# Kernel tuning notes

Hardware: AMD Instinct MI355X
Metric: run time of the kernel (lower is better)

The kernel has to match this reference:

```python
import jax, jax.numpy as jnp
import numpy as np

N_A, N_B = 30000, 30000
V, D_IN, D_OUT, H, E = 2, 128, 128, 4, 480000
EPS_LN = 1e-5


def setup_inputs() -> dict:
    key = jax.random.key(0)
    ks = jax.random.split(key, 22)
    rn = lambda i, sh, s=1.0: jax.random.normal(ks[i], sh, dtype=jnp.float32) * s
    ri = lambda i, n: jax.random.randint(ks[i], (E,), 0, n, dtype=jnp.int32)
    return {
        'feat_A': rn(0, (N_A, V, D_IN)),
        'feat_B': rn(1, (N_B, V, D_IN)),
        'src_ab': ri(2, N_A), 'dst_ab': ri(3, N_B),
        'val_ab': jax.random.uniform(ks[4], (E,), dtype=jnp.float32),
        'src_ba': ri(5, N_B), 'dst_ba': ri(6, N_A),
        'val_ba': jax.random.uniform(ks[7], (E,), dtype=jnp.float32),
        'W1': rn(8, (D_OUT, D_IN), 0.05), 'b1': jnp.zeros((D_OUT,), jnp.float32),
        'g1': jnp.ones((D_OUT,), jnp.float32), 'be1': jnp.zeros((D_OUT,), jnp.float32),
        'W2': rn(9, (D_OUT, D_IN), 0.05), 'b2': jnp.zeros((D_OUT,), jnp.float32),
        'g2': jnp.ones((D_OUT,), jnp.float32), 'be2': jnp.zeros((D_OUT,), jnp.float32),
        'Win': rn(10, (3 * D_OUT, D_OUT), 0.05), 'bin_': jnp.zeros((3 * D_OUT,), jnp.float32),
        'Wout': rn(11, (D_OUT, D_OUT), 0.05), 'bout': jnp.zeros((D_OUT,), jnp.float32),
        'lng': jnp.ones((D_OUT,), jnp.float32), 'lnb': jnp.zeros((D_OUT,), jnp.float32),
    }


def spmm_t(src, dst, val, h, n_out):
    # (adj^T @ h) over all views: h [N_src, V, d] -> [n_out, V, d]
    msg = h[src] * val[:, None, None]
    return jax.ops.segment_sum(msg, dst, num_segments=n_out)


def l2norm(x):
    n = jnp.sqrt(jnp.sum(x * x, axis=-1, keepdims=True))
    return x / jnp.maximum(n, 1e-12)


def layernorm(x, g, b):
    mu = jnp.mean(x, axis=-1, keepdims=True)
    var = jnp.mean((x - mu) ** 2, axis=-1, keepdims=True)
    return (x - mu) * jax.lax.rsqrt(var + EPS_LN) * g + b


def proj(x, W, b, g, be):
    # Linear -> LayerNorm -> ReLU
    return jax.nn.relu(layernorm(x @ W.T + b, g, be))


def mha(x, Win, bin_, Wout, bout, num_heads):
    # self-attention over the metapath axis P; x [..., P, d]
    *lead, P, d = x.shape
    dh = d // num_heads
    q, k, v = jnp.split(x @ Win.T + bin_, 3, axis=-1)
    hd = lambda t: t.reshape(*lead, P, num_heads, dh)
    q = hd(q) * (dh ** -0.5)
    scores = jnp.einsum('...qhe,...khe->...hqk', q, hd(k))
    a = jax.nn.softmax(scores, axis=-1)
    o = jnp.einsum('...hqk,...khe->...qhe', a, hd(v)).reshape(*lead, P, d)
    return o @ Wout.T + bout


def reference(feat_A, feat_B, src_ab, dst_ab, val_ab, src_ba, dst_ba, val_ba,
              W1, b1, g1, be1, W2, b2, g2, be2, Win, bin_, Wout, bout, lng, lnb):
    # metapath A->B->A
    h = l2norm(spmm_t(src_ab, dst_ab, val_ab, feat_A, N_B))
    h = l2norm(spmm_t(src_ba, dst_ba, val_ba, h, N_A))
    h1 = proj(h, W1, b1, g1, be1)                       # [N_A, V, d]
    # metapath B->A
    h = l2norm(spmm_t(src_ba, dst_ba, val_ba, feat_B, N_A))
    h2 = proj(h, W2, b2, g2, be2)                       # [N_A, V, d]
    x = jnp.stack([h1, h2], axis=2)                     # [N_A, V, P=2, d]
    attn = mha(x, Win, bin_, Wout, bout, H)
    y = layernorm(attn + x, lng, lnb).mean(axis=2)      # [N_A, V, d]
    return y  # h_global['A']; type B is identity passthrough of feat_B
```

## Files before the change

### kernel.cpp

```cpp
#include <hip/hip_runtime.h>

#define D 128
#define NODE_ROW 256
#define AP 8
#define AR (AP * 2)

typedef __attribute__((ext_vector_type(8))) short short8;
typedef __attribute__((ext_vector_type(4))) float floatx4;

__device__ __forceinline__ ushort f2bf(float f) {
    unsigned int u = __float_as_uint(f);
    u += 0x7fffu + ((u >> 16) & 1u);
    return (ushort)(u >> 16);
}
__device__ __forceinline__ unsigned int pk2(float a, float b) {
    return (unsigned int)f2bf(a) | ((unsigned int)f2bf(b) << 16);
}
__device__ __forceinline__ void up8(uint4 u, float* f) {
    f[0] = __uint_as_float(u.x << 16); f[1] = __uint_as_float(u.x & 0xffff0000u);
    f[2] = __uint_as_float(u.y << 16); f[3] = __uint_as_float(u.y & 0xffff0000u);
    f[4] = __uint_as_float(u.z << 16); f[5] = __uint_as_float(u.z & 0xffff0000u);
    f[6] = __uint_as_float(u.w << 16); f[7] = __uint_as_float(u.w & 0xffff0000u);
}
__device__ __forceinline__ float bf2f(ushort h) {
    return __uint_as_float(((unsigned int)h) << 16);
}
__device__ __forceinline__ short8 ldfrag(const ushort* p) {
    union { uint4 u; short8 s; } cv;
    cv.u = *(const uint4*)p;
    return cv.s;
}
__device__ __forceinline__ void acc4(float4& a, float w, uint2 u) {
    a.x += w * __uint_as_float(u.x << 16);
    a.y += w * __uint_as_float(u.x & 0xffff0000u);
    a.z += w * __uint_as_float(u.y << 16);
    a.w += w * __uint_as_float(u.y & 0xffff0000u);
}

__global__ __launch_bounds__(256) void k_f2b2(
    const float* __restrict__ srcA, const float* __restrict__ srcB,
    ushort* __restrict__ dstA, ushort* __restrict__ dstB, int n8) {
    int i = blockIdx.x * 256 + threadIdx.x;
    const float* s; ushort* d; int k;
    if (i < n8) { s = srcA; d = dstA; k = i; }
    else if (i < 2 * n8) { s = srcB; d = dstB; k = i - n8; }
    else return;
    const float4* sp = (const float4*)s + (size_t)k * 2;
    float4 a = sp[0], b = sp[1];
    uint4 o;
    o.x = pk2(a.x, a.y); o.y = pk2(a.z, a.w);
    o.z = pk2(b.x, b.y); o.w = pk2(b.z, b.w);
    ((uint4*)d)[k] = o;
}


__global__ __launch_bounds__(256) void k_hist(
    const int* __restrict__ dst_ab, const int* __restrict__ dst_ba,
    int* __restrict__ cnt_ab, int* __restrict__ cnt_ba, int E) {
    int i = blockIdx.x * 256 + threadIdx.x;
    if (i >= E) return;
    atomicAdd(&cnt_ab[dst_ab[i]], 1);
    atomicAdd(&cnt_ba[dst_ba[i]], 1);
}

__global__ __launch_bounds__(1024) void k_scan2(
    int* __restrict__ cntB, int* __restrict__ startB, int nB_,
    int* __restrict__ cntA, int* __restrict__ startA, int nA_) {
    __shared__ int part[1024];
    int* cnt; int* start; int n;
    if (blockIdx.x == 0) { cnt = cntB; start = startB; n = nB_; }
    else                 { cnt = cntA; start = startA; n = nA_; }
    int t = threadIdx.x;
    int chunk = (n + 1023) >> 10;
    int lo = min(t * chunk, n), hi = min(lo + chunk, n);
    int s = 0;
    for (int i = lo; i < hi; i++) s += cnt[i];
    part[t] = s;
    __syncthreads();
    for (int d = 1; d < 1024; d <<= 1) {
        int v = (t >= d) ? part[t - d] : 0;
        __syncthreads();
        part[t] += v;
        __syncthreads();
    }
    int off = part[t] - s;
    for (int i = lo; i < hi; i++) {
        int c = cnt[i];
        start[i] = off;
        cnt[i] = off;
        off += c;
    }
    if (t == 1023) start[n] = off;
}

__global__ __launch_bounds__(256) void k_scatter(
    const int* __restrict__ src_ab, const int* __restrict__ dst_ab,
    const float* __restrict__ val_ab,
    const int* __restrict__ src_ba, const int* __restrict__ dst_ba,
    const float* __restrict__ val_ba,
    int* __restrict__ cur_ab, int* __restrict__ cur_ba,
    int2* __restrict__ ep_ab, int2* __restrict__ ep_ba, int E) {
    int i = blockIdx.x * 256 + threadIdx.x;
    if (i >= E) return;
    {
        int pos = atomicAdd(&cur_ab[dst_ab[i]], 1);
        ep_ab[pos] = make_int2(src_ab[i], __float_as_int(val_ab[i]));
    }
    {
        int pos = atomicAdd(&cur_ba[dst_ba[i]], 1);
        ep_ba[pos] = make_int2(src_ba[i], __float_as_int(val_ba[i]));
    }
}


__global__ __launch_bounds__(256) void k_gather_norm_bf(
    const ushort* __restrict__ feat, const int2* __restrict__ ep,
    const int* __restrict__ start, ushort* __restrict__ out, int n) {
    int node = blockIdx.x * 4 + (threadIdx.x >> 6);
    if (node >= n) return;
    int lane = threadIdx.x & 63;
    int lo = start[node], hi = start[node + 1];
    float4 acc = make_float4(0.f, 0.f, 0.f, 0.f);
    int i = lo;
    for (; i + 3 < hi; i += 4) {
        int2 p0 = ep[i], p1 = ep[i + 1], p2 = ep[i + 2], p3 = ep[i + 3];
        uint2 u0 = ((const uint2*)(feat + (size_t)p0.x * NODE_ROW))[lane];
        uint2 u1 = ((const uint2*)(feat + (size_t)p1.x * NODE_ROW))[lane];
        uint2 u2 = ((const uint2*)(feat + (size_t)p2.x * NODE_ROW))[lane];
        uint2 u3 = ((const uint2*)(feat + (size_t)p3.x * NODE_ROW))[lane];
        acc4(acc, __int_as_float(p0.y), u0);
        acc4(acc, __int_as_float(p1.y), u1);
        acc4(acc, __int_as_float(p2.y), u2);
        acc4(acc, __int_as_float(p3.y), u3);
    }
    for (; i < hi; i++) {
        int2 p = ep[i];
        uint2 u = ((const uint2*)(feat + (size_t)p.x * NODE_ROW))[lane];
        acc4(acc, __int_as_float(p.y), u);
    }
    float ss = acc.x * acc.x + acc.y * acc.y + acc.z * acc.z + acc.w * acc.w;
    #pragma unroll
    for (int o = 16; o > 0; o >>= 1) ss += __shfl_xor(ss, o, 32);
    float sc = 1.0f / fmaxf(sqrtf(ss), 1e-12f);
    uint2 o;
    o.x = pk2(acc.x * sc, acc.y * sc);
    o.y = pk2(acc.z * sc, acc.w * sc);
    ((uint2*)(out + (size_t)node * NODE_ROW))[lane] = o;
}

__global__ __launch_bounds__(256) void k_gather2_bf(
    const ushort* __restrict__ featP, const ushort* __restrict__ featQ,
    const int2* __restrict__ ep, const int* __restrict__ start,
    ushort* __restrict__ outP, ushort* __restrict__ outQ, int n) {
    int node = blockIdx.x * 4 + (threadIdx.x >> 6);
    if (node >= n) return;
    int lane = threadIdx.x & 63;
    int lo = start[node], hi = start[node + 1];
    float4 aP = make_float4(0.f, 0.f, 0.f, 0.f);
    float4 aQ = make_float4(0.f, 0.f, 0.f, 0.f);
    int i = lo;
    for (; i + 3 < hi; i += 4) {
        int2 p0 = ep[i], p1 = ep[i + 1], p2 = ep[i + 2], p3 = ep[i + 3];
        size_t o0 = (size_t)p0.x * NODE_ROW, o1 = (size_t)p1.x * NODE_ROW;
        size_t o2 = (size_t)p2.x * NODE_ROW, o3 = (size_t)p3.x * NODE_ROW;
        uint2 uP0 = ((const uint2*)(featP + o0))[lane];
        uint2 uQ0 = ((const uint2*)(featQ + o0))[lane];
        uint2 uP1 = ((const uint2*)(featP + o1))[lane];
        uint2 uQ1 = ((const uint2*)(featQ + o1))[lane];
        uint2 uP2 = ((const uint2*)(featP + o2))[lane];
        uint2 uQ2 = ((const uint2*)(featQ + o2))[lane];
        uint2 uP3 = ((const uint2*)(featP + o3))[lane];
        uint2 uQ3 = ((const uint2*)(featQ + o3))[lane];
        float w0 = __int_as_float(p0.y), w1 = __int_as_float(p1.y);
        float w2 = __int_as_float(p2.y), w3 = __int_as_float(p3.y);
        acc4(aP, w0, uP0); acc4(aQ, w0, uQ0);
        acc4(aP, w1, uP1); acc4(aQ, w1, uQ1);
        acc4(aP, w2, uP2); acc4(aQ, w2, uQ2);
        acc4(aP, w3, uP3); acc4(aQ, w3, uQ3);
    }
    for (; i < hi; i++) {
        int2 p = ep[i];
        float w = __int_as_float(p.y);
        size_t off = (size_t)p.x * NODE_ROW;
        uint2 uP = ((const uint2*)(featP + off))[lane];
        uint2 uQ = ((const uint2*)(featQ + off))[lane];
        acc4(aP, w, uP); acc4(aQ, w, uQ);
    }
    uint2 oP, oQ;
    oP.x = pk2(aP.x, aP.y); oP.y = pk2(aP.z, aP.w);
    oQ.x = pk2(aQ.x, aQ.y); oQ.y = pk2(aQ.z, aQ.w);
    ((uint2*)(outP + (size_t)node * NODE_ROW))[lane] = oP;
    ((uint2*)(outQ + (size_t)node * NODE_ROW))[lane] = oQ;
}

__global__ __launch_bounds__(256) void k_cvt(
    const float* __restrict__ W1, const float* __restrict__ W2,
    const float* __restrict__ Win, const float* __restrict__ Wout,
    ushort* __restrict__ dst) {
    int idx = (blockIdx.x * 256 + threadIdx.x) * 4;
    if (idx >= 98304) return;
    const float* s; int off;
    if (idx < 16384)      { s = W1;  off = idx; }
    else if (idx < 32768) { s = W2;  off = idx - 16384; }
    else if (idx < 81920) { s = Win; off = idx - 32768; }
    else                  { s = Wout; off = idx - 81920; }
    float4 f = *(const float4*)(s + off);
    uint2 p;
    p.x = pk2(f.x, f.y);
    p.y = pk2(f.z, f.w);
    *(uint2*)(dst + idx) = p;
}

__global__ __launch_bounds__(128) void k_projm2(
    const ushort* __restrict__ in1, const ushort* __restrict__ Wb1,
    const float* __restrict__ b1, const float* __restrict__ g1,
    const float* __restrict__ be1,
    const ushort* __restrict__ in2, const ushort* __restrict__ Wb2,
    const float* __restrict__ b2, const float* __restrict__ g2,
    const float* __restrict__ be2,
    ushort* __restrict__ xbuf) {
    __shared__ ushort xn[16][136];
    __shared__ float yb[16][128];
    int p = blockIdx.y;
    const ushort* in = p ? in2 : in1;
    const ushort* Wb = p ? Wb2 : Wb1;
    const float*  b  = p ? b2  : b1;
    const float*  g  = p ? g2  : g1;
    const float*  be = p ? be2 : be1;
    int t = threadIdx.x;
    size_t rowbase = (size_t)blockIdx.x * 16;
    int r = t >> 3, i = t & 7;

    {
        const ushort* gp = in + (rowbase + r) * D + i * 16;
        float v[16];
        up8(((const uint4*)gp)[0], v);
        up8(((const uint4*)gp)[1], v + 8);
        float ss = 0.f;
        #pragma unroll
        for (int e = 0; e < 16; e++) ss += v[e] * v[e];
        ss += __shfl_xor(ss, 1, 8);
        ss += __shfl_xor(ss, 2, 8);
        ss += __shfl_xor(ss, 4, 8);
        float sc = 1.0f / fmaxf(sqrtf(ss), 1e-12f);
        uint4 w0, w1;
        w0.x = pk2(v[0]*sc, v[1]*sc);   w0.y = pk2(v[2]*sc, v[3]*sc);
        w0.z = pk2(v[4]*sc, v[5]*sc);   w0.w = pk2(v[6]*sc, v[7]*sc);
        w1.x = pk2(v[8]*sc, v[9]*sc);   w1.y = pk2(v[10]*sc, v[11]*sc);
        w1.z = pk2(v[12]*sc, v[13]*sc); w1.w = pk2(v[14]*sc, v[15]*sc);
        ushort* dst = &xn[r][i * 16];
        ((uint4*)dst)[0] = w0;
        ((uint4*)dst)[1] = w1;
    }
    __syncthreads();

    {
        int lane = t & 63, w = t >> 6, c = lane & 15, quad = lane >> 4;
        short8 af[4];
        #pragma unroll
        for (int kt = 0; kt < 4; kt++)
            af[kt] = ldfrag(&xn[c][kt * 32 + quad * 8]);
        #pragma unroll
        for (int nt2 = 0; nt2 < 4; nt2++) {
            int j = (w * 4 + nt2) * 16 + c;
            floatx4 acc = {0.f, 0.f, 0.f, 0.f};
            #pragma unroll
            for (int kt = 0; kt < 4; kt++) {
                short8 bfr = ldfrag(Wb + (size_t)j * 128 + kt * 32 + quad * 8);
                acc = __builtin_amdgcn_mfma_f32_16x16x32_bf16(af[kt], bfr, acc, 0, 0, 0);
            }
            float bj = b[j];
            #pragma unroll
            for (int rg = 0; rg < 4; rg++)
                yb[quad * 4 + rg][j] = acc[rg] + bj;
        }
    }
    __syncthreads();

    {
        float v[16];
        const float* yr = &yb[r][i * 16];
        #pragma unroll
        for (int e = 0; e < 16; e++) v[e] = yr[e];
        float s1 = 0.f, s2 = 0.f;
        #pragma unroll
        for (int e = 0; e < 16; e++) { s1 += v[e]; s2 += v[e] * v[e]; }
        s1 += __shfl_xor(s1, 1, 8); s2 += __shfl_xor(s2, 1, 8);
        s1 += __shfl_xor(s1, 2, 8); s2 += __shfl_xor(s2, 2, 8);
        s1 += __shfl_xor(s1, 4, 8); s2 += __shfl_xor(s2, 4, 8);
        float mu = s1 * (1.0f / 128.0f);
        float var = s2 * (1.0f / 128.0f) - mu * mu;
        float rs = rsqrtf(var + 1e-5f);
        const float* gg = g + i * 16;
        const float* bb = be + i * 16;
        float res[16];
        #pragma unroll
        for (int e = 0; e < 16; e++)
            res[e] = fmaxf((v[e] - mu) * rs * gg[e] + bb[e], 0.f);
        ushort* op = xbuf + ((rowbase + r) * 2 + p) * D + i * 16;
        uint4 w0, w1;
        w0.x = pk2(res[0], res[1]);   w0.y = pk2(res[2], res[3]);
        w0.z = pk2(res[4], res[5]);   w0.w = pk2(res[6], res[7]);
        w1.x = pk2(res[8], res[9]);   w1.y = pk2(res[10], res[11]);
        w1.z = pk2(res[12], res[13]); w1.w = pk2(res[14], res[15]);
        ((uint4*)op)[0] = w0;
        ((uint4*)op)[1] = w1;
    }
}

#define QKS 260
__global__ __launch_bounds__(256, 5) void k_attn2(
    const ushort* __restrict__ xbuf,
    const ushort* __restrict__ Winb, const float* __restrict__ binq,
    const ushort* __restrict__ Woutb, const float* __restrict__ bout,
    const float* __restrict__ lng, const float* __restrict__ lnb,
    float* __restrict__ out) {
    __shared__ ushort xb[AR][136];
    __shared__ float qk[AR][QKS];
    __shared__ ushort vb[AR][136];
    __shared__ ushort ob[AR][136];
    __shared__ float mu_s[AR], rs_s[AR];
    int t = threadIdx.x;
    int lane = t & 63, w = t >> 6;
    int c = lane & 15, quad = lane >> 4;
    size_t pairbase = (size_t)blockIdx.x * AP;
    size_t rowbase = pairbase * 2;

    const uint2* gx = (const uint2*)(xbuf + rowbase * D);
    #pragma unroll
    for (int i = t; i < AR * D / 4; i += 256) {
        int r = i >> 5;
        int col = (i & 31) * 4;
        *(uint2*)&xb[r][col] = gx[i];
    }
    __syncthreads();

    {
        short8 af[4];
        #pragma unroll
        for (int kt = 0; kt < 4; kt++)
            af[kt] = ldfrag(&xb[c][kt * 32 + quad * 8]);
        #pragma unroll
        for (int nt2 = 0; nt2 < 6; nt2++) {
            int j = (w * 6 + nt2) * 16 + c;
            floatx4 acc = {0.f, 0.f, 0.f, 0.f};
            #pragma unroll
            for (int kt = 0; kt < 4; kt++) {
                short8 bfr = ldfrag(Winb + (size_t)j * 128 + kt * 32 + quad * 8);
                acc = __builtin_amdgcn_mfma_f32_16x16x32_bf16(af[kt], bfr, acc, 0, 0, 0);
            }
            float bj = binq[j];
            if (j < 256) {
                float sc = (j < 128) ? 0.17677669529663687f : 1.0f;
                #pragma unroll
                for (int rg = 0; rg < 4; rg++)
                    qk[quad * 4 + rg][j] = (acc[rg] + bj) * sc;
            } else {
                #pragma unroll
                for (int rg = 0; rg < 4; rg++)
                    vb[quad * 4 + rg][j - 256] = f2bf(acc[rg] + bj);
            }
        }
    }
    __syncthreads();

    {
        int half = t & 1, kk = (t >> 1) & 1, pq = (t >> 2) & 1;
        int h = (t >> 3) & 3, pp = t >> 5;
        int qrow = 2 * pp + pq;
        const float4* qp = (const float4*)&qk[qrow][h * 32 + half * 16];
        const float4* kp = (const float4*)&qk[2 * pp + kk][128 + h * 32 + half * 16];
        float s = 0.f;
        #pragma unroll
        for (int m = 0; m < 4; m++) {
            float4 qv = qp[m], kv = kp[m];
            s += qv.x * kv.x + qv.y * kv.y + qv.z * kv.z + qv.w * kv.w;
        }
        s += __shfl_xor(s, 1, 64);
        float so = __shfl_xor(s, 2, 64);
        float s0 = kk ? so : s;
        float s1 = kk ? s : so;
        float m0 = fmaxf(s0, s1);
        float e0 = __expf(s0 - m0), e1 = __expf(s1 - m0);
        float inv = 1.f / (e0 + e1);
        float a0 = e0 * inv, a1 = e1 * inv;
        int cbase = h * 32 + kk * 16 + half * 8;
        const uint2* v0p = (const uint2*)&vb[2 * pp][cbase];
        const uint2* v1p = (const uint2*)&vb[2 * pp + 1][cbase];
        ushort* op = &ob[qrow][cbase];
        #pragma unroll
        for (int m = 0; m < 2; m++) {
            uint2 u0 = v0p[m], u1 = v1p[m];
            float o0 = a0 * __uint_as_float(u0.x << 16)         + a1 * __uint_as_float(u1.x << 16);
            float o1 = a0 * __uint_as_float(u0.x & 0xffff0000u) + a1 * __uint_as_float(u1.x & 0xffff0000u);
            float o2 = a0 * __uint_as_float(u0.y << 16)         + a1 * __uint_as_float(u1.y << 16);
            float o3 = a0 * __uint_as_float(u0.y & 0xffff0000u) + a1 * __uint_as_float(u1.y & 0xffff0000u);
            uint2 pw;
            pw.x = pk2(o0, o1); pw.y = pk2(o2, o3);
            ((uint2*)op)[m] = pw;
        }
    }
    __syncthreads();

    {
        short8 af[4];
        #pragma unroll
        for (int kt = 0; kt < 4; kt++)
            af[kt] = ldfrag(&ob[c][kt * 32 + quad * 8]);
        #pragma unroll
        for (int nt2 = 0; nt2 < 2; nt2++) {
            int j = (w * 2 + nt2) * 16 + c;
            floatx4 acc = {0.f, 0.f, 0.f, 0.f};
            #pragma unroll
            for (int kt = 0; kt < 4; kt++) {
                short8 bfr = ldfrag(Woutb + (size_t)j * 128 + kt * 32 + quad * 8);
                acc = __builtin_amdgcn_mfma_f32_16x16x32_bf16(af[kt], bfr, acc, 0, 0, 0);
            }
            float bj = bout[j];
            #pragma unroll
            for (int rg = 0; rg < 4; rg++) {
                int row = quad * 4 + rg;
                qk[row][j] = acc[rg] + bj + bf2f(xb[row][j]);
            }
        }
    }
    __syncthreads();

    if (t < 128) {
        int r = t >> 3, i = t & 7;
        float s1 = 0.f, s2 = 0.f;
        const float* yr = &qk[r][i * 16];
        #pragma unroll
        for (int cc = 0; cc < 16; cc++) { float v = yr[cc]; s1 += v; s2 += v * v; }
        s1 += __shfl_down(s1, 4, 8); s2 += __shfl_down(s2, 4, 8);
        s1 += __shfl_down(s1, 2, 8); s2 += __shfl_down(s2, 2, 8);
        s1 += __shfl_down(s1, 1, 8); s2 += __shfl_down(s2, 1, 8);
        if (i == 0) {
            float mu = s1 / D;
            float var = s2 / D - mu * mu;
            mu_s[r] = mu; rs_s[r] = rsqrtf(var + 1e-5f);
        }
    }
    __syncthreads();

    if (t < 128) {
        int j = t;
        float gj = lng[j], bj = lnb[j];
        #pragma unroll
        for (int pp = 0; pp < AP; pp++) {
            int r0 = pp * 2, r1 = r0 + 1;
            float v0 = (qk[r0][j] - mu_s[r0]) * rs_s[r0] * gj + bj;
            float v1 = (qk[r1][j] - mu_s[r1]) * rs_s[r1] * gj + bj;
            out[(pairbase + pp) * D + j] = 0.5f * (v0 + v1);
        }
    }
}

extern "C" void kernel_launch(void* const* d_in, const int* in_sizes, int n_in,
                              void* d_out, int out_size, void* d_ws, size_t ws_size,
                              hipStream_t stream) {
    const float* feat_A = (const float*)d_in[0];
    const float* feat_B = (const float*)d_in[1];
    const int*   src_ab = (const int*)d_in[2];
    const int*   dst_ab = (const int*)d_in[3];
    const float* val_ab = (const float*)d_in[4];
    const int*   src_ba = (const int*)d_in[5];
    const int*   dst_ba = (const int*)d_in[6];
    const float* val_ba = (const float*)d_in[7];
    const float* W1 = (const float*)d_in[8];
    const float* b1 = (const float*)d_in[9];
    const float* g1 = (const float*)d_in[10];
    const float* be1 = (const float*)d_in[11];
    const float* W2 = (const float*)d_in[12];
    const float* b2 = (const float*)d_in[13];
    const float* g2 = (const float*)d_in[14];
    const float* be2 = (const float*)d_in[15];
    const float* Win = (const float*)d_in[16];
    const float* binq = (const float*)d_in[17];
    const float* Wout = (const float*)d_in[18];
    const float* bout = (const float*)d_in[19];
    const float* lng = (const float*)d_in[20];
    const float* lnb = (const float*)d_in[21];

    int E  = in_sizes[2];
    int nA = in_sizes[0] / NODE_ROW;
    int nB = in_sizes[1] / NODE_ROW;
    int rowsA = nA * 2;
    size_t nodeElems = (size_t)nA * NODE_ROW;

    ushort* fbA  = (ushort*)d_ws;
    ushort* fbB  = fbA + nodeElems;
    ushort* hB   = fbB + nodeElems;
    ushort* hA1  = hB + nodeElems;
    ushort* hA2  = hA1 + nodeElems;
    ushort* xbuf = hA2 + nodeElems;
    ushort* Wbf  = xbuf + (size_t)rowsA * 2 * D;
    ushort* W1b   = Wbf;
    ushort* W2b   = Wbf + 16384;
    ushort* Winb  = Wbf + 32768;
    ushort* Woutb = Wbf + 81920;
    int* cnt_ab   = (int*)(Wbf + 98304);
    int* cnt_ba   = cnt_ab + nB;
    int* start_ab = cnt_ba + nA;
    int* start_ba = start_ab + (nB + 1);
    uintptr_t a = (uintptr_t)(start_ba + (nA + 1));
    a = (a + 15) & ~(uintptr_t)15;
    int2* ep_ab = (int2*)a;
    int2* ep_ba = ep_ab + E;

    int egrid = (E + 255) / 256;
    int n8 = (int)(nodeElems / 8);

    k_f2b2<<<(2 * n8 + 255) / 256, 256, 0, stream>>>(feat_A, feat_B, fbA, fbB, n8);

    hipMemsetAsync(cnt_ab, 0, (size_t)(nA + nB) * sizeof(int), stream);
    k_hist<<<egrid, 256, 0, stream>>>(dst_ab, dst_ba, cnt_ab, cnt_ba, E);
    k_scan2<<<2, 1024, 0, stream>>>(cnt_ab, start_ab, nB, cnt_ba, start_ba, nA);
    k_scatter<<<egrid, 256, 0, stream>>>(src_ab, dst_ab, val_ab,
                                         src_ba, dst_ba, val_ba,
                                         cnt_ab, cnt_ba, ep_ab, ep_ba, E);

    k_cvt<<<96, 256, 0, stream>>>(W1, W2, Win, Wout, Wbf);

    k_gather_norm_bf<<<(nB + 3) / 4, 256, 0, stream>>>(fbA, ep_ab, start_ab, hB, nB);
    k_gather2_bf<<<(nA + 3) / 4, 256, 0, stream>>>(hB, fbB, ep_ba, start_ba,
                                                   hA1, hA2, nA);

    k_projm2<<<dim3(rowsA / 16, 2), 128, 0, stream>>>(hA1, W1b, b1, g1, be1,
                                                      hA2, W2b, b2, g2, be2, xbuf);
    k_attn2<<<rowsA / AP, 256, 0, stream>>>(xbuf, Winb, binq, Woutb, bout,
                                            lng, lnb, (float*)d_out);
}
```

Before: 560.7 us.

## Fuse attention scores and softmax into QKV MFMA registers in k_attn2

Each wave now computes the Q, K and V column tiles for the same head-aligned 32 columns, so the attention scores, the two-way softmax and the weighted sum over V are done directly from the MFMA accumulators with shuffle reductions. This removes the qk and vb shared staging buffers and one block barrier. The smaller shared-memory footprint allows a higher launch-bounds occupancy target (6 instead of 5). The cost is more live registers and extra cross-lane shuffles. V is also no longer rounded to bf16 before the weighted sum.

```diff
diff --git a/kernel.cpp b/kernel.cpp
--- a/kernel.cpp
+++ b/kernel.cpp
@@ -308,17 +308,15 @@
     }
 }
 
-#define QKS 260
-__global__ __launch_bounds__(256, 5) void k_attn2(
+__global__ __launch_bounds__(256, 6) void k_attn2(
     const ushort* __restrict__ xbuf,
     const ushort* __restrict__ Winb, const float* __restrict__ binq,
     const ushort* __restrict__ Woutb, const float* __restrict__ bout,
     const float* __restrict__ lng, const float* __restrict__ lnb,
     float* __restrict__ out) {
     __shared__ ushort xb[AR][136];
-    __shared__ float qk[AR][QKS];
-    __shared__ ushort vb[AR][136];
-    __shared__ ushort ob[AR][136];
+    __shared__ ushort obuf[AR][140];
+    __shared__ float yy[AR][132];
     __shared__ float mu_s[AR], rs_s[AR];
     int t = threadIdx.x;
     int lane = t & 63, w = t >> 6;
@@ -340,64 +338,66 @@
         #pragma unroll
         for (int kt = 0; kt < 4; kt++)
             af[kt] = ldfrag(&xb[c][kt * 32 + quad * 8]);
-        #pragma unroll
-        for (int nt2 = 0; nt2 < 6; nt2++) {
-            int j = (w * 6 + nt2) * 16 + c;
-            floatx4 acc = {0.f, 0.f, 0.f, 0.f};
+        floatx4 aq0 = {0.f,0.f,0.f,0.f}, aq1 = {0.f,0.f,0.f,0.f};
+        floatx4 ak0 = {0.f,0.f,0.f,0.f}, ak1 = {0.f,0.f,0.f,0.f};
+        floatx4 av0 = {0.f,0.f,0.f,0.f}, av1 = {0.f,0.f,0.f,0.f};
+        int jb = w * 32 + c;
+        #pragma unroll
+        for (int kt = 0; kt < 4; kt++) {
+            const ushort* wp = Winb + kt * 32 + quad * 8;
+            short8 f0 = ldfrag(wp + (size_t)(jb)       * 128);
+            short8 f1 = ldfrag(wp + (size_t)(jb + 16)  * 128);
+            short8 f2 = ldfrag(wp + (size_t)(jb + 128) * 128);
+            short8 f3 = ldfrag(wp + (size_t)(jb + 144) * 128);
+            short8 f4 = ldfrag(wp + (size_t)(jb + 256) * 128);
+            short8 f5 = ldfrag(wp + (size_t)(jb + 272) * 128);
+            aq0 = __builtin_amdgcn_mfma_f32_16x16x32_bf16(af[kt], f0, aq0, 0, 0, 0);
+            aq1 = __builtin_amdgcn_mfma_f32_16x16x32_bf16(af[kt], f1, aq1, 0, 0, 0);
+            ak0 = __builtin_amdgcn_mfma_f32_16x16x32_bf16(af[kt], f2, ak0, 0, 0, 0);
+            ak1 = __builtin_amdgcn_mfma_f32_16x16x32_bf16(af[kt], f3, ak1, 0, 0, 0);
+            av0 = __builtin_amdgcn_mfma_f32_16x16x32_bf16(af[kt], f4, av0, 0, 0, 0);
+            av1 = __builtin_amdgcn_mfma_f32_16x16x32_bf16(af[kt], f5, av1, 0, 0, 0);
+        }
+        const float qs = 0.17677669529663687f;
+        float bq0 = binq[jb] ;        float bq1 = binq[jb + 16];
+        float bk0 = binq[jb + 128];   float bk1 = binq[jb + 144];
+        float bv0 = binq[jb + 256];   float bv1 = binq[jb + 272];
+        #pragma unroll
+        for (int rg = 0; rg < 4; rg++) {
+            aq0[rg] = (aq0[rg] + bq0) * qs;
+            aq1[rg] = (aq1[rg] + bq1) * qs;
+            ak0[rg] += bk0;  ak1[rg] += bk1;
+            av0[rg] += bv0;  av1[rg] += bv1;
+        }
+        #pragma unroll
+        for (int pl = 0; pl < 2; pl++) {
+            int r0 = 2 * pl, r1 = 2 * pl + 1;
+            float p00 = aq0[r0] * ak0[r0] + aq1[r0] * ak1[r0];
+            float p01 = aq0[r0] * ak0[r1] + aq1[r0] * ak1[r1];
+            float p10 = aq0[r1] * ak0[r0] + aq1[r1] * ak1[r0];
+            float p11 = aq0[r1] * ak0[r1] + aq1[r1] * ak1[r1];
             #pragma unroll
-            for (int kt = 0; kt < 4; kt++) {
-                short8 bfr = ldfrag(Winb + (size_t)j * 128 + kt * 32 + quad * 8);
-                acc = __builtin_amdgcn_mfma_f32_16x16x32_bf16(af[kt], bfr, acc, 0, 0, 0);
+            for (int m = 1; m < 16; m <<= 1) {
+                p00 += __shfl_xor(p00, m, 16);
+                p01 += __shfl_xor(p01, m, 16);
+                p10 += __shfl_xor(p10, m, 16);
+                p11 += __shfl_xor(p11, m, 16);
             }
-            float bj = binq[j];
-            if (j < 256) {
-                float sc = (j < 128) ? 0.17677669529663687f : 1.0f;
-                #pragma unroll
-                for (int rg = 0; rg < 4; rg++)
-                    qk[quad * 4 + rg][j] = (acc[rg] + bj) * sc;
-            } else {
-                #pragma unroll
-                for (int rg = 0; rg < 4; rg++)
-                    vb[quad * 4 + rg][j - 256] = f2bf(acc[rg] + bj);
-            }
-        }
-    }
-    __syncthreads();
-
-    {
-        int half = t & 1, kk = (t >> 1) & 1, pq = (t >> 2) & 1;
-        int h = (t >> 3) & 3, pp = t >> 5;
-        int qrow = 2 * pp + pq;
-        const float4* qp = (const float4*)&qk[qrow][h * 32 + half * 16];
-        const float4* kp = (const float4*)&qk[2 * pp + kk][128 + h * 32 + half * 16];
-        float s = 0.f;
-        #pragma unroll
-        for (int m = 0; m < 4; m++) {
-            float4 qv = qp[m], kv = kp[m];
-            s += qv.x * kv.x + qv.y * kv.y + qv.z * kv.z + qv.w * kv.w;
-        }
-        s += __shfl_xor(s, 1, 64);
-        float so = __shfl_xor(s, 2, 64);
-        float s0 = kk ? so : s;
-        float s1 = kk ? s : so;
-        float m0 = fmaxf(s0, s1);
-        float e0 = __expf(s0 - m0), e1 = __expf(s1 - m0);
-        float inv = 1.f / (e0 + e1);
-        float a0 = e0 * inv, a1 = e1 * inv;
-        int cbase = h * 32 + kk * 16 + half * 8;
-        const uint2* v0p = (const uint2*)&vb[2 * pp][cbase];
-        const uint2* v1p = (const uint2*)&vb[2 * pp + 1][cbase];
-        ushort* op = &ob[qrow][cbase];
-        #pragma unroll
-        for (int m = 0; m < 2; m++) {
-            uint2 u0 = v0p[m], u1 = v1p[m];
-            float o0 = a0 * __uint_as_float(u0.x << 16)         + a1 * __uint_as_float(u1.x << 16);
-            float o1 = a0 * __uint_as_float(u0.x & 0xffff0000u) + a1 * __uint_as_float(u1.x & 0xffff0000u);
-            float o2 = a0 * __uint_as_float(u0.y << 16)         + a1 * __uint_as_float(u1.y << 16);
-            float o3 = a0 * __uint_as_float(u0.y & 0xffff0000u) + a1 * __uint_as_float(u1.y & 0xffff0000u);
-            uint2 pw;
-            pw.x = pk2(o0, o1); pw.y = pk2(o2, o3);
-            ((uint2*)op)[m] = pw;
+            float mx0 = fmaxf(p00, p01), mx1 = fmaxf(p10, p11);
+            float e00 = __expf(p00 - mx0), e01 = __expf(p01 - mx0);
+            float e10 = __expf(p10 - mx1), e11 = __expf(p11 - mx1);
+            float i0 = 1.f / (e00 + e01), i1 = 1.f / (e10 + e11);
+            float a00 = e00 * i0, a01 = e01 * i0;
+            float a10 = e10 * i1, a11 = e11 * i1;
+            float o00 = a00 * av0[r0] + a01 * av0[r1];
+            float o10 = a10 * av0[r0] + a11 * av0[r1];
+            float o01 = a00 * av1[r0] + a01 * av1[r1];
+            float o11 = a10 * av1[r0] + a11 * av1[r1];
+            int row0 = quad * 4 + r0, row1 = quad * 4 + r1;
+            obuf[row0][jb]      = f2bf(o00);
+            obuf[row1][jb]      = f2bf(o10);
+            obuf[row0][jb + 16] = f2bf(o01);
+            obuf[row1][jb + 16] = f2bf(o11);
         }
     }
     __syncthreads();
@@ -406,7 +406,7 @@
         short8 af[4];
         #pragma unroll
         for (int kt = 0; kt < 4; kt++)
-            af[kt] = ldfrag(&ob[c][kt * 32 + quad * 8]);
+            af[kt] = ldfrag(&obuf[c][kt * 32 + quad * 8]);
         #pragma unroll
         for (int nt2 = 0; nt2 < 2; nt2++) {
             int j = (w * 2 + nt2) * 16 + c;
@@ -420,7 +420,7 @@
             #pragma unroll
             for (int rg = 0; rg < 4; rg++) {
                 int row = quad * 4 + rg;
-                qk[row][j] = acc[rg] + bj + bf2f(xb[row][j]);
+                yy[row][j] = acc[rg] + bj + bf2f(xb[row][j]);
             }
         }
     }
@@ -429,7 +429,7 @@
     if (t < 128) {
         int r = t >> 3, i = t & 7;
         float s1 = 0.f, s2 = 0.f;
-        const float* yr = &qk[r][i * 16];
+        const float* yr = &yy[r][i * 16];
         #pragma unroll
         for (int cc = 0; cc < 16; cc++) { float v = yr[cc]; s1 += v; s2 += v * v; }
         s1 += __shfl_down(s1, 4, 8); s2 += __shfl_down(s2, 4, 8);
@@ -449,8 +449,8 @@
         #pragma unroll
         for (int pp = 0; pp < AP; pp++) {
             int r0 = pp * 2, r1 = r0 + 1;
-            float v0 = (qk[r0][j] - mu_s[r0]) * rs_s[r0] * gj + bj;
-            float v1 = (qk[r1][j] - mu_s[r1]) * rs_s[r1] * gj + bj;
+            float v0 = (yy[r0][j] - mu_s[r0]) * rs_s[r0] * gj + bj;
+            float v1 = (yy[r1][j] - mu_s[r1]) * rs_s[r1] * gj + bj;
             out[(pairbase + pp) * D + j] = 0.5f * (v0 + v1);
         }
     }
```

Result: no change. 567.9 us (+1.3%).
